# Kernel tuning notes

Hardware: AMD Instinct MI355X
Metric: run time of the kernel (lower is better)

Reference implementation:

```python
import jax, jax.numpy as jnp
import numpy as np

N = 2048
MAX_ITER = 1000          # hardcoded in XGR.forward (max_iter=1000)
TOL = 1e-6               # symmetric_sinkhorn default tol
WEIGHT_LOSS_XGR = 250.0  # init kwarg weight_loss_XGR


def setup_inputs() -> dict:
    key = jax.random.key(0)
    k1, k2 = jax.random.split(key)
    A = jax.random.normal(k1, (N, N), dtype=jnp.float32)
    M = jnp.abs(A + A.T)  # symmetric, non-negative cost matrix
    group = jax.random.uniform(k2, (N, N), dtype=jnp.float32,
                               minval=1e-3, maxval=1.0)  # positive (log taken)
    return {"M": M, "group": group, "eps": 1}


def reference(M, group, eps):
    eps = jnp.asarray(eps, M.dtype)
    n = M.shape[0]

    def converged(f):
        # rows of log_T = (f_i + f_j - C_ij)/eps must sum (in prob domain) to 1
        log_T = (f[:, None] + f[None, :] - M) / eps
        row_sums = jnp.exp(jax.nn.logsumexp(log_T, axis=-1))
        return jnp.all(jnp.abs(row_sums - 1.0) < TOL)

    def cond_fn(state):
        _, k, done = state
        return jnp.logical_and(k < MAX_ITER, jnp.logical_not(done))

    def body_fn(state):
        f, k, _ = state
        # torch: f = 0.5*(f - eps*logsumexp((f - C)/eps, -1)); f broadcasts over rows
        f = 0.5 * (f - eps * jax.nn.logsumexp((f[None, :] - M) / eps, axis=-1))
        done = jax.lax.cond(k % 10 == 0, converged,
                            lambda _: jnp.array(False), f)
        return (f, k + 1, done)

    f0 = jnp.zeros((n,), dtype=M.dtype)
    f, _, _ = jax.lax.while_loop(cond_fn, body_fn,
                                 (f0, jnp.int32(0), jnp.array(False)))

    log_Q = (f[:, None] + f[None, :] - M) / eps
    loss = (group * (jnp.log(group) - log_Q - 1.0) + jnp.exp(log_Q)).sum()
    return WEIGHT_LOSS_XGR * loss
```

## Files before the change

### kernel.cpp

```cpp
#include <hip/hip_runtime.h>
#include <hip/hip_cooperative_groups.h>
#include <math.h>

namespace cg = cooperative_groups;

#define NN 2048
#define MAX_ITER 1000
#define TOLF 1e-6f
#define TPB 512
#define NBLK 256
#define WPB 8
#define SPIN_LIMIT (1 << 14)
#define LDS_SPIN_LIMIT (1 << 18)
#define FLAG_ABORT 0x7f000000

__device__ __forceinline__ unsigned long long pack_pair(unsigned int tag,
                                                        unsigned int viol,
                                                        float v) {
    return ((unsigned long long)((tag << 1) | viol) << 32) | (unsigned long long)__float_as_uint(v);
}

__global__ __launch_bounds__(TPB, 1)
void xgr_sinkhorn(const float* __restrict__ Mm,
                  const float* __restrict__ Gg,
                  const int* __restrict__ eps_p,
                  float* __restrict__ out,
                  unsigned long long* __restrict__ ws64)
{
    __shared__ float  m_lds[WPB][NN];
    __shared__ float  fA[NN], fB[NN];
    __shared__ int    sflag[2][WPB];
    __shared__ double s_part[WPB];

    unsigned long long* gb0 = ws64;
    unsigned long long* gb1 = ws64 + NN;
    double*       acc      = (double*)(ws64 + 2 * NN);
    unsigned int* done_cnt = (unsigned int*)(ws64 + 2 * NN + 1);
    unsigned int* abortp   = done_cnt + 1;

    const int tid  = threadIdx.x;
    const int lane = tid & 63;
    const int wave = tid >> 6;
    const int row  = blockIdx.x * WPB + wave;
    const int gtid = blockIdx.x * TPB + tid;

    if (tid < WPB) {
        const int r = blockIdx.x * WPB + tid;
        gb0[r] = 0ULL;
        gb1[r] = 0xFFFFFFFF00000000ULL;
    }
    if (gtid == 0) { *acc = 0.0; *done_cnt = 0u; *abortp = 0u; }
    if (tid < 2 * WPB) ((int*)sflag)[tid] = -1;

    const int ebits = *eps_p;
    const float eps = (ebits >= 1 && ebits <= (1 << 20)) ? (float)ebits
                                                         : __int_as_float(ebits);
    const float inv_eps = 1.0f / eps;

    {
        const float4* Mrow = (const float4*)(Mm + (size_t)row * NN);
        float4* ml4 = (float4*)m_lds[wave];
        #pragma unroll
        for (int k = 0; k < 8; ++k) {
            const int idx = (k << 6) + lane;
            ml4[idx] = Mrow[idx];
        }
    }

    cg::this_grid().sync();

    float* f_final = nullptr;
    bool   aborted = false;

    for (int t = 0; ; ++t) {
        const int p = t & 1;
        float* fl = p ? fB : fA;
        unsigned long long* gb  = p ? gb1 : gb0;
        unsigned long long* gbn = p ? gb0 : gb1;

        {
            const unsigned int want = (unsigned int)t;
            unsigned long long* gw = gb + (wave << 8) + (lane << 2);
            unsigned long long pw0 = 0, pw1 = 0, pw2 = 0, pw3 = 0;
            bool ok0 = false, ok1 = false, ok2 = false, ok3 = false;
            int vio = 0, guard = 0;
            for (;;) {
                if (!ok0) { unsigned long long q = __hip_atomic_load(gw + 0, __ATOMIC_RELAXED, __HIP_MEMORY_SCOPE_AGENT);
                            if ((unsigned int)(q >> 33) == want) { ok0 = true; pw0 = q; vio |= (int)((q >> 32) & 1ULL); } }
                if (!ok1) { unsigned long long q = __hip_atomic_load(gw + 1, __ATOMIC_RELAXED, __HIP_MEMORY_SCOPE_AGENT);
                            if ((unsigned int)(q >> 33) == want) { ok1 = true; pw1 = q; vio |= (int)((q >> 32) & 1ULL); } }
                if (!ok2) { unsigned long long q = __hip_atomic_load(gw + 2, __ATOMIC_RELAXED, __HIP_MEMORY_SCOPE_AGENT);
                            if ((unsigned int)(q >> 33) == want) { ok2 = true; pw2 = q; vio |= (int)((q >> 32) & 1ULL); } }
                if (!ok3) { unsigned long long q = __hip_atomic_load(gw + 3, __ATOMIC_RELAXED, __HIP_MEMORY_SCOPE_AGENT);
                            if ((unsigned int)(q >> 33) == want) { ok3 = true; pw3 = q; vio |= (int)((q >> 32) & 1ULL); } }
                if (__all(ok0 && ok1 && ok2 && ok3)) break;
                if ((++guard & 63) == 0) {
                    int ab = 0;
                    if (lane == 0) ab = (int)__hip_atomic_load(abortp, __ATOMIC_RELAXED, __HIP_MEMORY_SCOPE_AGENT);
                    ab = __shfl(ab, 0);
                    if (ab || guard > SPIN_LIMIT) {
                        if (lane == 0) __hip_atomic_store(abortp, 1u, __ATOMIC_RELAXED, __HIP_MEMORY_SCOPE_AGENT);
                        aborted = true; break;
                    }
                }
            }
            float4 v;
            v.x = __uint_as_float((unsigned int)pw0);
            v.y = __uint_as_float((unsigned int)pw1);
            v.z = __uint_as_float((unsigned int)pw2);
            v.w = __uint_as_float((unsigned int)pw3);
            ((float4*)(fl + (wave << 8)))[lane] = v;
            const int wv = __any(vio != 0) ? 1 : 0;
            __threadfence_block();
            if (lane == 0)
                *(volatile int*)&sflag[p][wave] = aborted ? FLAG_ABORT : ((t << 1) | wv);
        }
        if (aborted) { f_final = fl; break; }

        float x[32];
        float mloc = -INFINITY;
        int violall = 0;
        const float4* ml4 = (const float4*)m_lds[wave];
        for (int c = 0; c < WPB; ++c) {
            volatile int* fp = &sflag[p][c];
            int v = *fp;
            int g = 0;
            while (v < (t << 1)) {
                __builtin_amdgcn_s_sleep(1);
                if ((++g & 1023) == 0) {
                    int ab = 0;
                    if (lane == 0) ab = (int)__hip_atomic_load(abortp, __ATOMIC_RELAXED, __HIP_MEMORY_SCOPE_AGENT);
                    ab = __shfl(ab, 0);
                    if (ab || g > LDS_SPIN_LIMIT) { aborted = true; break; }
                }
                v = *fp;
            }
            if (aborted || v >= FLAG_ABORT) { aborted = true; break; }
            violall |= (v & 1);
            const float4 f4 = ((const float4*)(fl + (c << 8)))[lane];
            const float4 mv = ml4[(c << 6) + lane];
            const float x0 = (f4.x - mv.x) * inv_eps;
            const float x1 = (f4.y - mv.y) * inv_eps;
            const float x2 = (f4.z - mv.z) * inv_eps;
            const float x3 = (f4.w - mv.w) * inv_eps;
            x[4*c+0] = x0; x[4*c+1] = x1; x[4*c+2] = x2; x[4*c+3] = x3;
            mloc = fmaxf(mloc, fmaxf(fmaxf(x0, x1), fmaxf(x2, x3)));
        }
        if (aborted) {
            if (lane == 0) __hip_atomic_store(abortp, 1u, __ATOMIC_RELAXED, __HIP_MEMORY_SCOPE_AGENT);
            f_final = fl; break;
        }

        if ((t % 10) == 2 && violall == 0) {
            f_final = p ? fA : fB;
            break;
        }
        if (t == MAX_ITER) { f_final = fl; break; }

        float mw = mloc;
        #pragma unroll
        for (int off = 32; off; off >>= 1)
            mw = fmaxf(mw, __shfl_down(mw, off));
        mw = __shfl(mw, 0);
        float s = 0.0f;
        #pragma unroll
        for (int k = 0; k < 32; ++k) s += expf(x[k] - mw);
        #pragma unroll
        for (int off = 32; off; off >>= 1)
            s += __shfl_down(s, off);

        if (lane == 0) {
            const float L  = mw + logf(s);
            const float fi = fl[row];
            const float fn = 0.5f * (fi - eps * L);
            unsigned int viol = 0u;
            if ((t % 10) == 1) {
                const float rs = expf(fi * inv_eps + L);
                viol = (fabsf(rs - 1.0f) < TOLF) ? 0u : 1u;
            }
            __hip_atomic_store(&gbn[row], pack_pair((unsigned int)(t + 1), viol, fn),
                               __ATOMIC_RELAXED, __HIP_MEMORY_SCOPE_AGENT);
        }
    }

    __syncthreads();
    const float4* Grow = (const float4*)(Gg + (size_t)row * NN);
    const float4* ml4  = (const float4*)m_lds[wave];
    const float4* fl4  = (const float4*)f_final;
    const float   fi   = f_final[row];
    double lsum = 0.0;
    #pragma unroll
    for (int k = 0; k < 8; ++k) {
        const int idx = (k << 6) + lane;
        const float4 mv = ml4[idx];
        const float4 gv = Grow[idx];
        const float4 f4 = fl4[idx];
        {
            const float lq = (fi + f4.x - mv.x) * inv_eps;
            lsum += (double)(gv.x * (logf(gv.x) - lq - 1.0f) + expf(lq));
        }
        {
            const float lq = (fi + f4.y - mv.y) * inv_eps;
            lsum += (double)(gv.y * (logf(gv.y) - lq - 1.0f) + expf(lq));
        }
        {
            const float lq = (fi + f4.z - mv.z) * inv_eps;
            lsum += (double)(gv.z * (logf(gv.z) - lq - 1.0f) + expf(lq));
        }
        {
            const float lq = (fi + f4.w - mv.w) * inv_eps;
            lsum += (double)(gv.w * (logf(gv.w) - lq - 1.0f) + expf(lq));
        }
    }
    #pragma unroll
    for (int off = 32; off; off >>= 1)
        lsum += __shfl_down(lsum, off);

    if (lane == 0) s_part[wave] = lsum;
    __syncthreads();
    if (tid == 0) {
        double b = 0.0;
        #pragma unroll
        for (int w = 0; w < WPB; ++w) b += s_part[w];
        atomicAdd(acc, b);
        __threadfence();
        const unsigned int prev = __hip_atomic_fetch_add(done_cnt, 1u,
                                                         __ATOMIC_RELAXED, __HIP_MEMORY_SCOPE_AGENT);
        if (prev == NBLK - 1) {
            __threadfence();
            const double total = __hip_atomic_load(acc, __ATOMIC_RELAXED,
                                                   __HIP_MEMORY_SCOPE_AGENT);
            out[0] = (float)(250.0 * total);
        }
    }
}

extern "C" void kernel_launch(void* const* d_in, const int* in_sizes, int n_in,
                              void* d_out, int out_size, void* d_ws, size_t ws_size,
                              hipStream_t stream)
{
    const float* Mm    = (const float*)d_in[0];
    const float* Gg    = (const float*)d_in[1];
    const int*   eps_p = (const int*)d_in[2];
    float* out = (float*)d_out;
    unsigned long long* ws64 = (unsigned long long*)d_ws;

    void* args[] = { (void*)&Mm, (void*)&Gg, (void*)&eps_p, (void*)&out, (void*)&ws64 };
    hipLaunchCooperativeKernel((void*)xgr_sinkhorn, dim3(NBLK), dim3(TPB),
                               args, 0, stream);
}
```

Measured before the change: 298.5 us.

## Replicate global f broadcast buffers per block group to spread polling traffic

```diff
diff --git a/kernel.cpp b/kernel.cpp
--- a/kernel.cpp
+++ b/kernel.cpp
@@ -10,6 +10,7 @@
 #define TPB 512
 #define NBLK 256
 #define WPB 8
+#define NREP 8
 #define SPIN_LIMIT (1 << 14)
 #define LDS_SPIN_LIMIT (1 << 18)
 #define FLAG_ABORT 0x7f000000
@@ -32,10 +33,8 @@
     __shared__ int    sflag[2][WPB];
     __shared__ double s_part[WPB];
 
-    unsigned long long* gb0 = ws64;
-    unsigned long long* gb1 = ws64 + NN;
-    double*       acc      = (double*)(ws64 + 2 * NN);
-    unsigned int* done_cnt = (unsigned int*)(ws64 + 2 * NN + 1);
+    double*       acc      = (double*)(ws64 + NREP * 2 * NN);
+    unsigned int* done_cnt = (unsigned int*)(acc + 1);
     unsigned int* abortp   = done_cnt + 1;
 
     const int tid  = threadIdx.x;
@@ -43,11 +42,13 @@
     const int wave = tid >> 6;
     const int row  = blockIdx.x * WPB + wave;
     const int gtid = blockIdx.x * TPB + tid;
-
-    if (tid < WPB) {
-        const int r = blockIdx.x * WPB + tid;
-        gb0[r] = 0ULL;
-        gb1[r] = 0xFFFFFFFF00000000ULL;
+    const int grp  = blockIdx.x >> 5;
+
+    if (tid < NREP * 2 * WPB) {
+        const int rep = tid >> 4, p = (tid >> 3) & 1, rw = tid & 7;
+        const int r = blockIdx.x * WPB + rw;
+        ws64[(rep * 2 + p) * NN + r] = p ? 0xFFFFFFFF00000000ULL
+                                         : 0ULL;
     }
     if (gtid == 0) { *acc = 0.0; *done_cnt = 0u; *abortp = 0u; }
     if (tid < 2 * WPB) ((int*)sflag)[tid] = -1;
@@ -75,8 +76,7 @@
     for (int t = 0; ; ++t) {
         const int p = t & 1;
         float* fl = p ? fB : fA;
-        unsigned long long* gb  = p ? gb1 : gb0;
-        unsigned long long* gbn = p ? gb0 : gb1;
+        unsigned long long* gb = ws64 + (grp * 2 + p) * NN;
 
         {
             const unsigned int want = (unsigned int)t;
@@ -94,6 +94,7 @@
                 if (!ok3) { unsigned long long q = __hip_atomic_load(gw + 3, __ATOMIC_RELAXED, __HIP_MEMORY_SCOPE_AGENT);
                             if ((unsigned int)(q >> 33) == want) { ok3 = true; pw3 = q; vio |= (int)((q >> 32) & 1ULL); } }
                 if (__all(ok0 && ok1 && ok2 && ok3)) break;
+                __builtin_amdgcn_s_sleep(1);
                 if ((++guard & 63) == 0) {
                     int ab = 0;
                     if (lane == 0) ab = (int)__hip_atomic_load(abortp, __ATOMIC_RELAXED, __HIP_MEMORY_SCOPE_AGENT);
@@ -121,7 +122,8 @@
         float mloc = -INFINITY;
         int violall = 0;
         const float4* ml4 = (const float4*)m_lds[wave];
-        for (int c = 0; c < WPB; ++c) {
+        for (int j = 0; j < WPB; ++j) {
+            const int c = (wave + j) & 7;
             volatile int* fp = &sflag[p][c];
             int v = *fp;
             int g = 0;
@@ -178,8 +180,12 @@
                 const float rs = expf(fi * inv_eps + L);
                 viol = (fabsf(rs - 1.0f) < TOLF) ? 0u : 1u;
             }
-            __hip_atomic_store(&gbn[row], pack_pair((unsigned int)(t + 1), viol, fn),
-                               __ATOMIC_RELAXED, __HIP_MEMORY_SCOPE_AGENT);
+            const unsigned long long w = pack_pair((unsigned int)(t + 1), viol, fn);
+            const int pn = (t + 1) & 1;
+            #pragma unroll
+            for (int r = 0; r < NREP; ++r)
+                __hip_atomic_store(ws64 + (r * 2 + pn) * NN + row, w,
+                                   __ATOMIC_RELAXED, __HIP_MEMORY_SCOPE_AGENT);
         }
     }
 
```

Result: slower. 466.0 us (+56.1%).
